# Optimization experiments

Measured on AMD Instinct MI355X. Metric: run time of the kernel, lower is better.

Reference implementation:

```python
import jax, jax.numpy as jnp
import numpy as np

NUM_VOCAB = 50000
EMBED_DIM = 128
SENT_SIZE = 50
MAX_HOPS = 3
BATCH = 128
MEM_SIZE = 200


def position_encoding(sentence_size, embedding_dim):
    # vectorized version of the original double loop
    i = np.arange(1, embedding_dim + 1, dtype=np.float32)[:, None]  # [D,1]
    j = np.arange(1, sentence_size + 1, dtype=np.float32)[None, :]  # [1,S]
    enc = (i - (embedding_dim + 1) / 2.0) * (j - (sentence_size + 1) / 2.0)
    enc = 1.0 + 4.0 * enc / embedding_dim / sentence_size
    enc[:, -1] = 1.0
    return np.transpose(enc).astype(np.float32)  # [S,D]


def setup_inputs() -> dict:
    key = jax.random.key(0)
    k1, k2, k3, k4, k5 = jax.random.split(key, 5)
    story = jax.random.randint(k1, (BATCH, MEM_SIZE, SENT_SIZE), 0, NUM_VOCAB, dtype=jnp.int64)
    query = jax.random.randint(k2, (BATCH, SENT_SIZE), 0, NUM_VOCAB, dtype=jnp.int64)
    # max_hops+1 embedding tables, N(0, 0.1), padding_idx=0 row zeroed
    C = 0.1 * jax.random.normal(k3, (MAX_HOPS + 1, NUM_VOCAB, EMBED_DIM), dtype=jnp.float32)
    C = C.at[:, 0, :].set(0.0)
    # T_k linear layer (PyTorch default uniform init bound)
    bound = 1.0 / np.sqrt(EMBED_DIM)
    T_w = jax.random.uniform(k4, (EMBED_DIM, EMBED_DIM), jnp.float32, -bound, bound)
    T_b = jax.random.uniform(k5, (EMBED_DIM,), jnp.float32, -bound, bound)
    return {"story": story, "query": query, "C": C, "T_w": T_w, "T_b": T_b}


def reference(story, query, C, T_w, T_b):
    enc = jnp.asarray(position_encoding(SENT_SIZE, EMBED_DIM))  # [S,D]
    # u0: position-encoded sum of query embedding
    q_emb = C[0][query]  # [B,S,D]
    u = jnp.einsum('bsd,sd->bd', q_emb, enc)
    for hop in range(MAX_HOPS):
        emb_A = C[hop][story]          # [B,M,S,D]
        m_A = jnp.einsum('bmsd,sd->bmd', emb_A, enc)
        prob = jax.nn.softmax(jnp.einsum('bmd,bd->bm', m_A, u), axis=-1)
        emb_C = C[hop + 1][story]      # [B,M,S,D]
        m_C = jnp.einsum('bmsd,sd->bmd', emb_C, enc)
        o_k = jnp.einsum('bmd,bm->bd', m_C, prob)
        t_k = jax.nn.sigmoid(u @ T_w.T + T_b)
        u = (1.0 - t_k) * u + o_k * t_k
    a_hat = u @ C[MAX_HOPS].T  # [B,V]
    return a_hat
```

## Files before the change

kernel.cpp:

```cpp
#include <hip/hip_runtime.h>
#include <cstdint>
#include <cstddef>

#define NV 50000
#define ED 128
#define SS 50
#define NB 128
#define NM 200
#define BMD (NB*NM*ED)
#define NCH 32
#define CHD 1563

typedef _Float16 f16x8 __attribute__((ext_vector_type(8)));
typedef _Float16 f16x4 __attribute__((ext_vector_type(4)));
typedef _Float16 f16x2 __attribute__((ext_vector_type(2)));
typedef float    f32x4 __attribute__((ext_vector_type(4)));

__global__ __launch_bounds__(256) void cvt_c3_k(
    const float* __restrict__ src, _Float16* __restrict__ dst) {
  const int i = blockIdx.x * 256 + threadIdx.x;
  const float4* s4 = (const float4*)src;
  float4 f0 = s4[2 * (size_t)i];
  float4 f1 = s4[2 * (size_t)i + 1];
  f16x8 h;
  h[0] = (_Float16)f0.x; h[1] = (_Float16)f0.y;
  h[2] = (_Float16)f0.z; h[3] = (_Float16)f0.w;
  h[4] = (_Float16)f1.x; h[5] = (_Float16)f1.y;
  h[6] = (_Float16)f1.z; h[7] = (_Float16)f1.w;
  *(f16x8*)(dst + (size_t)8 * i) = h;
}

__global__ __launch_bounds__(256) void story_embed_k(
    const int* __restrict__ story, const float* __restrict__ C,
    const _Float16* __restrict__ C3h, float* __restrict__ Mt) {
  const int wave = threadIdx.x >> 6;
  const int lane = threadIdx.x & 63;
  const int bm0 = blockIdx.x * 16;
  const int sl = (lane < SS) ? lane : (SS - 1);

  int idxg[4], cidg[4];
#pragma unroll
  for (int gg = 0; gg < 4; ++gg) {
    const int bm = bm0 + wave + 4 * gg;
    idxg[gg] = story[(size_t)bm * SS + sl];
    cidg[gg] = (lane < SS) ? (idxg[gg] / CHD) : -1;
  }
  const float a0 = ((float)(2*lane + 1) - 64.5f) * 6.25e-4f;
  const float a1 = ((float)(2*lane + 2) - 64.5f) * 6.25e-4f;
  float2 acc[4][4];
#pragma unroll
  for (int gg = 0; gg < 4; ++gg)
#pragma unroll
    for (int k = 0; k < 4; ++k) acc[gg][k] = make_float2(0.f, 0.f);

  for (int c = 0; c < NCH; ++c) {
#pragma unroll
    for (int gg = 0; gg < 4; ++gg) {
      unsigned long long mask = __ballot(cidg[gg] == c);
      while (mask) {
        const int s = __builtin_ctzll(mask);
        mask &= mask - 1;
        const int row = __shfl(idxg[gg], s);
        float e0, e1;
        if (s == SS - 1) { e0 = 1.0f; e1 = 1.0f; }
        else {
          float js = (float)(s + 1) - 25.5f;
          e0 = fmaf(a0, js, 1.0f);
          e1 = fmaf(a1, js, 1.0f);
        }
        const float* base = C + (size_t)row * ED + 2 * lane;
#pragma unroll
        for (int k = 0; k < 3; ++k) {
          float2 cv = *(const float2*)(base + (size_t)k * NV * ED);
          acc[gg][k].x = fmaf(e0, cv.x, acc[gg][k].x);
          acc[gg][k].y = fmaf(e1, cv.y, acc[gg][k].y);
        }
        f16x2 cv3 = *(const f16x2*)(C3h + (size_t)row * ED + 2 * lane);
        acc[gg][3].x = fmaf(e0, (float)cv3[0], acc[gg][3].x);
        acc[gg][3].y = fmaf(e1, (float)cv3[1], acc[gg][3].y);
      }
    }
    __syncthreads();
  }

#pragma unroll
  for (int gg = 0; gg < 4; ++gg) {
    const int bm = bm0 + wave + 4 * gg;
#pragma unroll
    for (int k = 0; k < 4; ++k)
      *(float2*)(Mt + (size_t)k * BMD + (size_t)bm * ED + 2 * lane) = acc[gg][k];
  }
}

__global__ __launch_bounds__(512, 2) void hops_k(
    const int* __restrict__ query, const float* __restrict__ C,
    const float* __restrict__ Tw, const float* __restrict__ Tb,
    const float* __restrict__ Mt, float* __restrict__ U) {
  const int b = blockIdx.x;
  const int tid = threadIdx.x;
  const int d = tid & 127;
  const int p = tid >> 7;
  const int wave = tid >> 6, lane = tid & 63;
  __shared__ float tile[NM * ED];
  __shared__ float u[ED];
  __shared__ float part[512];
  __shared__ float sc[NM];
  __shared__ float o[ED];

  {
    const float4* s4 = (const float4*)(Mt + (size_t)b * NM * ED);
    float4* t4 = (float4*)tile;
    float4 st[13];
#pragma unroll
    for (int j = 0; j < 13; ++j) {
      int i = tid + 512 * j;
      st[j] = (i < NM * ED / 4) ? s4[i] : make_float4(0.f, 0.f, 0.f, 0.f);
    }
#pragma unroll
    for (int j = 0; j < 13; ++j) {
      int i = tid + 512 * j;
      if (i < NM * ED / 4) t4[i] = st[j];
    }
  }

  {
    const float ad = ((float)(d + 1) - 64.5f) * 6.25e-4f;
    int rows[13];
#pragma unroll
    for (int j = 0; j < 13; ++j) {
      int s = p + 4 * j;
      rows[j] = query[b * SS + (s < SS ? s : 0)];
    }
    float cv[13];
#pragma unroll
    for (int j = 0; j < 13; ++j)
      cv[j] = C[(size_t)rows[j] * ED + d];
    float accv = 0.f;
#pragma unroll
    for (int j = 0; j < 13; ++j) {
      int s = p + 4 * j;
      float e;
      if (s >= SS) e = 0.f;
      else if (s == SS - 1) e = 1.0f;
      else e = fmaf(ad, (float)(s + 1) - 25.5f, 1.0f);
      accv = fmaf(e, cv[j], accv);
    }
    part[tid] = accv;
  }
  __syncthreads();
  if (tid < ED)
    u[tid] = part[tid] + part[tid + 128] + part[tid + 256] + part[tid + 384];
  __syncthreads();

  for (int hop = 0; hop < 3; ++hop) {
    const float* Tn = Mt + (size_t)(hop + 1) * BMD + (size_t)b * NM * ED;
    float pf[50];
#pragma unroll
    for (int j = 0; j < 50; ++j)
      pf[j] = Tn[(size_t)(p + 4 * j) * ED + d];

    {
      float u0v = u[2 * lane], u1v = u[2 * lane + 1];
      for (int m = wave; m < NM; m += 16) {
        const int m2 = m + 8;
        const bool has2 = (m2 < NM);
        float2 r0 = *(const float2*)&tile[m * ED + 2 * lane];
        float pa = r0.x * u0v + r0.y * u1v;
        float pb = 0.f;
        if (has2) {
          float2 r1 = *(const float2*)&tile[m2 * ED + 2 * lane];
          pb = r1.x * u0v + r1.y * u1v;
        }
#pragma unroll
        for (int off = 32; off; off >>= 1) {
          pa += __shfl_xor(pa, off);
          pb += __shfl_xor(pb, off);
        }
        if (lane == 0) {
          sc[m] = pa;
          if (has2) sc[m2] = pb;
        }
      }
    }
    __syncthreads();

    float v = (tid < NM) ? sc[tid] : -1e30f;
    {
      float t = v;
#pragma unroll
      for (int off = 32; off; off >>= 1) t = fmaxf(t, __shfl_xor(t, off));
      if (lane == 0) part[wave] = t;
    }
    __syncthreads();
    float mx = part[0];
#pragma unroll
    for (int w = 1; w < 8; ++w) mx = fmaxf(mx, part[w]);
    float ev = 0.f;
    if (tid < NM) { ev = __expf(v - mx); sc[tid] = ev; }
    {
      float t = ev;
#pragma unroll
      for (int off = 32; off; off >>= 1) t += __shfl_xor(t, off);
      if (lane == 0) part[8 + wave] = t;
    }
    __syncthreads();
    float tot = part[8];
#pragma unroll
    for (int w = 9; w < 16; ++w) tot += part[w];
    const float inv = 1.0f / tot;
    __syncthreads();

    {
      float oacc = 0.f;
#pragma unroll
      for (int j = 0; j < 50; ++j)
        oacc = fmaf(sc[p + 4 * j], pf[j], oacc);
      part[tid] = oacc;
    }
    if (hop < 2) {
#pragma unroll
      for (int j = 0; j < 50; ++j)
        tile[(p + 4 * j) * ED + d] = pf[j];
    }
    __syncthreads();
    if (tid < ED)
      o[tid] = (part[tid] + part[tid + 128] + part[tid + 256] + part[tid + 384])
               * inv;
    __syncthreads();

    {
      const float4* twr = (const float4*)(Tw + (size_t)d * ED + p * 32);
      float4 tw4[8];
#pragma unroll
      for (int j = 0; j < 8; ++j) tw4[j] = twr[j];
      float tacc = 0.f;
#pragma unroll
      for (int j = 0; j < 8; ++j) {
        tacc = fmaf(u[p * 32 + 4 * j + 0], tw4[j].x, tacc);
        tacc = fmaf(u[p * 32 + 4 * j + 1], tw4[j].y, tacc);
        tacc = fmaf(u[p * 32 + 4 * j + 2], tw4[j].z, tacc);
        tacc = fmaf(u[p * 32 + 4 * j + 3], tw4[j].w, tacc);
      }
      part[tid] = tacc;
    }
    __syncthreads();
    if (tid < ED) {
      float dot = part[tid] + part[tid + 128] + part[tid + 256] + part[tid + 384]
                  + Tb[tid];
      float tk = 1.0f / (1.0f + __expf(-dot));
      u[tid] = (1.0f - tk) * u[tid] + o[tid] * tk;
    }
    __syncthreads();
  }
  if (tid < ED) U[(size_t)b * ED + tid] = u[tid];
}

__global__ __launch_bounds__(256) void out_mm_mfma_k(
    const float* __restrict__ U, const _Float16* __restrict__ C3h,
    float* __restrict__ out) {
  __shared__ _Float16 Ub[ED * 136];
  const int tid = threadIdx.x;

  {
    const float4* u4 = (const float4*)U;
#pragma unroll
    for (int j = 0; j < 16; ++j) {
      int i = tid + 256 * j;
      float4 f = u4[i];
      int row = i >> 5;
      int col = (i & 31) * 4;
      f16x4 h;
      h[0] = (_Float16)f.x; h[1] = (_Float16)f.y;
      h[2] = (_Float16)f.z; h[3] = (_Float16)f.w;
      *(f16x4*)&Ub[row * 136 + col] = h;
    }
  }
  __syncthreads();

  const int wave = tid >> 6, lane = tid & 63;
  const int n = lane & 15, q = lane >> 4;
  const int v = blockIdx.x * 64 + wave * 16 + n;
  const bool vok = (v < NV);

  f32x4 acc[8];
#pragma unroll
  for (int mt = 0; mt < 8; ++mt) acc[mt] = (f32x4){0.f, 0.f, 0.f, 0.f};

#pragma unroll
  for (int kt = 0; kt < 4; ++kt) {
    f16x8 bfrag = {};
    if (vok) bfrag = *(const f16x8*)(C3h + (size_t)v * ED + kt * 32 + q * 8);
#pragma unroll
    for (int mt = 0; mt < 8; ++mt) {
      f16x8 afrag = *(const f16x8*)&Ub[(mt * 16 + n) * 136 + kt * 32 + q * 8];
      acc[mt] = __builtin_amdgcn_mfma_f32_16x16x32_f16(afrag, bfrag, acc[mt],
                                                       0, 0, 0);
    }
  }

  if (vok) {
#pragma unroll
    for (int mt = 0; mt < 8; ++mt)
#pragma unroll
      for (int i = 0; i < 4; ++i)
        out[(size_t)(mt * 16 + q * 4 + i) * NV + v] = acc[mt][i];
  }
}

extern "C" void kernel_launch(void* const* d_in, const int* in_sizes, int n_in,
                              void* d_out, int out_size, void* d_ws, size_t ws_size,
                              hipStream_t stream) {
  const int*   story = (const int*)d_in[0];
  const int*   query = (const int*)d_in[1];
  const float* C     = (const float*)d_in[2];
  const float* Tw    = (const float*)d_in[3];
  const float* Tb    = (const float*)d_in[4];
  float* out = (float*)d_out;

  float* wsf = (float*)d_ws;
  float*     Mt  = wsf;
  float*     U   = wsf + (size_t)4 * BMD;
  _Float16*  C3h = (_Float16*)(wsf + (size_t)4 * BMD + NB * ED);

  hipLaunchKernelGGL(cvt_c3_k, dim3(NV * ED / 8 / 256), dim3(256), 0, stream,
                     C + (size_t)3 * NV * ED, C3h);
  hipLaunchKernelGGL(story_embed_k, dim3(NB * NM / 16), dim3(256), 0, stream,
                     story, C, C3h, Mt);
  hipLaunchKernelGGL(hops_k, dim3(NB), dim3(512), 0, stream,
                     query, C, Tw, Tb, Mt, U);
  hipLaunchKernelGGL(out_mm_mfma_k, dim3((NV + 63) / 64), dim3(256), 0, stream,
                     U, C3h, out);
}
```

Measured before the change: 359.9 us.

## Process two gathered story rows per iteration and widen hops kernel to 1024 threads

The story embedding gather loop now pops two matching lanes from the ballot mask per iteration and issues both rows' loads before the FMAs, raising memory-level parallelism in this latency-bound gather. The hops kernel doubles its block to 1024 threads, halving per-thread register arrays (pf, tile staging) and the per-thread work in each reduction, with the partial sums now reduced over 8 slices. The cost is more register pressure in the gather loop and only one 1024-thread block per CU for hops, which has just 128 blocks anyway.

```diff
diff --git a/kernel.cpp b/kernel.cpp
--- a/kernel.cpp
+++ b/kernel.cpp
@@ -58,26 +58,48 @@
     for (int gg = 0; gg < 4; ++gg) {
       unsigned long long mask = __ballot(cidg[gg] == c);
       while (mask) {
-        const int s = __builtin_ctzll(mask);
+        const int s0 = __builtin_ctzll(mask);
         mask &= mask - 1;
-        const int row = __shfl(idxg[gg], s);
-        float e0, e1;
-        if (s == SS - 1) { e0 = 1.0f; e1 = 1.0f; }
+        const bool two = (mask != 0);
+        int s1 = s0;
+        if (two) { s1 = __builtin_ctzll(mask); mask &= mask - 1; }
+        const int row0 = __shfl(idxg[gg], s0);
+        const int row1 = __shfl(idxg[gg], s1);
+        float e00, e01, e10, e11;
+        if (s0 == SS - 1) { e00 = 1.0f; e01 = 1.0f; }
         else {
-          float js = (float)(s + 1) - 25.5f;
-          e0 = fmaf(a0, js, 1.0f);
-          e1 = fmaf(a1, js, 1.0f);
-        }
-        const float* base = C + (size_t)row * ED + 2 * lane;
+          float js = (float)(s0 + 1) - 25.5f;
+          e00 = fmaf(a0, js, 1.0f);
+          e01 = fmaf(a1, js, 1.0f);
+        }
+        if (!two) { e10 = 0.f; e11 = 0.f; }
+        else if (s1 == SS - 1) { e10 = 1.0f; e11 = 1.0f; }
+        else {
+          float js = (float)(s1 + 1) - 25.5f;
+          e10 = fmaf(a0, js, 1.0f);
+          e11 = fmaf(a1, js, 1.0f);
+        }
+        const float* b0 = C + (size_t)row0 * ED + 2 * lane;
+        const float* b1 = C + (size_t)row1 * ED + 2 * lane;
+        float2 cv0[3], cv1[3];
 #pragma unroll
         for (int k = 0; k < 3; ++k) {
-          float2 cv = *(const float2*)(base + (size_t)k * NV * ED);
-          acc[gg][k].x = fmaf(e0, cv.x, acc[gg][k].x);
-          acc[gg][k].y = fmaf(e1, cv.y, acc[gg][k].y);
-        }
-        f16x2 cv3 = *(const f16x2*)(C3h + (size_t)row * ED + 2 * lane);
-        acc[gg][3].x = fmaf(e0, (float)cv3[0], acc[gg][3].x);
-        acc[gg][3].y = fmaf(e1, (float)cv3[1], acc[gg][3].y);
+          cv0[k] = *(const float2*)(b0 + (size_t)k * NV * ED);
+          cv1[k] = *(const float2*)(b1 + (size_t)k * NV * ED);
+        }
+        f16x2 h0 = *(const f16x2*)(C3h + (size_t)row0 * ED + 2 * lane);
+        f16x2 h1 = *(const f16x2*)(C3h + (size_t)row1 * ED + 2 * lane);
+#pragma unroll
+        for (int k = 0; k < 3; ++k) {
+          acc[gg][k].x = fmaf(e00, cv0[k].x, acc[gg][k].x);
+          acc[gg][k].y = fmaf(e01, cv0[k].y, acc[gg][k].y);
+          acc[gg][k].x = fmaf(e10, cv1[k].x, acc[gg][k].x);
+          acc[gg][k].y = fmaf(e11, cv1[k].y, acc[gg][k].y);
+        }
+        acc[gg][3].x = fmaf(e00, (float)h0[0], acc[gg][3].x);
+        acc[gg][3].y = fmaf(e01, (float)h0[1], acc[gg][3].y);
+        acc[gg][3].x = fmaf(e10, (float)h1[0], acc[gg][3].x);
+        acc[gg][3].y = fmaf(e11, (float)h1[1], acc[gg][3].y);
       }
     }
     __syncthreads();
@@ -92,7 +114,7 @@
   }
 }
 
-__global__ __launch_bounds__(512, 2) void hops_k(
+__global__ __launch_bounds__(1024, 1) void hops_k(
     const int* __restrict__ query, const float* __restrict__ C,
     const float* __restrict__ Tw, const float* __restrict__ Tb,
     const float* __restrict__ Mt, float* __restrict__ U) {
@@ -103,42 +125,42 @@
   const int wave = tid >> 6, lane = tid & 63;
   __shared__ float tile[NM * ED];
   __shared__ float u[ED];
-  __shared__ float part[512];
+  __shared__ float part[1024];
   __shared__ float sc[NM];
   __shared__ float o[ED];
 
   {
     const float4* s4 = (const float4*)(Mt + (size_t)b * NM * ED);
     float4* t4 = (float4*)tile;
-    float4 st[13];
-#pragma unroll
-    for (int j = 0; j < 13; ++j) {
-      int i = tid + 512 * j;
-      st[j] = (i < NM * ED / 4) ? s4[i] : make_float4(0.f, 0.f, 0.f, 0.f);
-    }
-#pragma unroll
-    for (int j = 0; j < 13; ++j) {
-      int i = tid + 512 * j;
+    float4 st[7];
+#pragma unroll
+    for (int j = 0; j < 7; ++j) {
+      int i = tid + 1024 * j;
+      if (i < NM * ED / 4) st[j] = s4[i];
+    }
+#pragma unroll
+    for (int j = 0; j < 7; ++j) {
+      int i = tid + 1024 * j;
       if (i < NM * ED / 4) t4[i] = st[j];
     }
   }
 
   {
     const float ad = ((float)(d + 1) - 64.5f) * 6.25e-4f;
-    int rows[13];
-#pragma unroll
-    for (int j = 0; j < 13; ++j) {
-      int s = p + 4 * j;
+    int rows[7];
+#pragma unroll
+    for (int j = 0; j < 7; ++j) {
+      int s = p + 8 * j;
       rows[j] = query[b * SS + (s < SS ? s : 0)];
     }
-    float cv[13];
-#pragma unroll
-    for (int j = 0; j < 13; ++j)
+    float cv[7];
+#pragma unroll
+    for (int j = 0; j < 7; ++j)
       cv[j] = C[(size_t)rows[j] * ED + d];
     float accv = 0.f;
 #pragma unroll
-    for (int j = 0; j < 13; ++j) {
-      int s = p + 4 * j;
+    for (int j = 0; j < 7; ++j) {
+      int s = p + 8 * j;
       float e;
       if (s >= SS) e = 0.f;
       else if (s == SS - 1) e = 1.0f;
@@ -148,21 +170,25 @@
     part[tid] = accv;
   }
   __syncthreads();
-  if (tid < ED)
-    u[tid] = part[tid] + part[tid + 128] + part[tid + 256] + part[tid + 384];
+  if (tid < ED) {
+    float s = 0.f;
+#pragma unroll
+    for (int k = 0; k < 8; ++k) s += part[tid + 128 * k];
+    u[tid] = s;
+  }
   __syncthreads();
 
   for (int hop = 0; hop < 3; ++hop) {
     const float* Tn = Mt + (size_t)(hop + 1) * BMD + (size_t)b * NM * ED;
-    float pf[50];
-#pragma unroll
-    for (int j = 0; j < 50; ++j)
-      pf[j] = Tn[(size_t)(p + 4 * j) * ED + d];
+    float pf[25];
+#pragma unroll
+    for (int j = 0; j < 25; ++j)
+      pf[j] = Tn[(size_t)(p + 8 * j) * ED + d];
 
     {
       float u0v = u[2 * lane], u1v = u[2 * lane + 1];
-      for (int m = wave; m < NM; m += 16) {
-        const int m2 = m + 8;
+      for (int m = wave; m < NM; m += 32) {
+        const int m2 = m + 16;
         const bool has2 = (m2 < NM);
         float2 r0 = *(const float2*)&tile[m * ED + 2 * lane];
         float pa = r0.x * u0v + r0.y * u1v;
@@ -194,59 +220,63 @@
     __syncthreads();
     float mx = part[0];
 #pragma unroll
-    for (int w = 1; w < 8; ++w) mx = fmaxf(mx, part[w]);
+    for (int w = 1; w < 16; ++w) mx = fmaxf(mx, part[w]);
     float ev = 0.f;
     if (tid < NM) { ev = __expf(v - mx); sc[tid] = ev; }
     {
       float t = ev;
 #pragma unroll
       for (int off = 32; off; off >>= 1) t += __shfl_xor(t, off);
-      if (lane == 0) part[8 + wave] = t;
-    }
-    __syncthreads();
-    float tot = part[8];
-#pragma unroll
-    for (int w = 9; w < 16; ++w) tot += part[w];
+      if (lane == 0) part[16 + wave] = t;
+    }
+    __syncthreads();
+    float tot = part[16];
+#pragma unroll
+    for (int w = 17; w < 32; ++w) tot += part[w];
     const float inv = 1.0f / tot;
     __syncthreads();
 
     {
       float oacc = 0.f;
 #pragma unroll
-      for (int j = 0; j < 50; ++j)
-        oacc = fmaf(sc[p + 4 * j], pf[j], oacc);
+      for (int j = 0; j < 25; ++j)
+        oacc = fmaf(sc[p + 8 * j], pf[j], oacc);
       part[tid] = oacc;
     }
     if (hop < 2) {
 #pragma unroll
-      for (int j = 0; j < 50; ++j)
-        tile[(p + 4 * j) * ED + d] = pf[j];
-    }
-    __syncthreads();
-    if (tid < ED)
-      o[tid] = (part[tid] + part[tid + 128] + part[tid + 256] + part[tid + 384])
-               * inv;
-    __syncthreads();
-
-    {
-      const float4* twr = (const float4*)(Tw + (size_t)d * ED + p * 32);
-      float4 tw4[8];
-#pragma unroll
-      for (int j = 0; j < 8; ++j) tw4[j] = twr[j];
+      for (int j = 0; j < 25; ++j)
+        tile[(p + 8 * j) * ED + d] = pf[j];
+    }
+    __syncthreads();
+    if (tid < ED) {
+      float s = 0.f;
+#pragma unroll
+      for (int k = 0; k < 8; ++k) s += part[tid + 128 * k];
+      o[tid] = s * inv;
+    }
+    __syncthreads();
+
+    {
+      const float4* twr = (const float4*)(Tw + (size_t)d * ED + p * 16);
+      float4 tw4[4];
+#pragma unroll
+      for (int j = 0; j < 4; ++j) tw4[j] = twr[j];
       float tacc = 0.f;
 #pragma unroll
-      for (int j = 0; j < 8; ++j) {
-        tacc = fmaf(u[p * 32 + 4 * j + 0], tw4[j].x, tacc);
-        tacc = fmaf(u[p * 32 + 4 * j + 1], tw4[j].y, tacc);
-        tacc = fmaf(u[p * 32 + 4 * j + 2], tw4[j].z, tacc);
-        tacc = fmaf(u[p * 32 + 4 * j + 3], tw4[j].w, tacc);
+      for (int j = 0; j < 4; ++j) {
+        tacc = fmaf(u[p * 16 + 4 * j + 0], tw4[j].x, tacc);
+        tacc = fmaf(u[p * 16 + 4 * j + 1], tw4[j].y, tacc);
+        tacc = fmaf(u[p * 16 + 4 * j + 2], tw4[j].z, tacc);
+        tacc = fmaf(u[p * 16 + 4 * j + 3], tw4[j].w, tacc);
       }
       part[tid] = tacc;
     }
     __syncthreads();
     if (tid < ED) {
-      float dot = part[tid] + part[tid + 128] + part[tid + 256] + part[tid + 384]
-                  + Tb[tid];
+      float dot = Tb[tid];
+#pragma unroll
+      for (int k = 0; k < 8; ++k) dot += part[tid + 128 * k];
       float tk = 1.0f / (1.0f + __expf(-dot));
       u[tid] = (1.0f - tk) * u[tid] + o[tid] * tk;
     }
@@ -326,7 +356,7 @@
                      C + (size_t)3 * NV * ED, C3h);
   hipLaunchKernelGGL(story_embed_k, dim3(NB * NM / 16), dim3(256), 0, stream,
                      story, C, C3h, Mt);
-  hipLaunchKernelGGL(hops_k, dim3(NB), dim3(512), 0, stream,
+  hipLaunchKernelGGL(hops_k, dim3(NB), dim3(1024), 0, stream,
                      query, C, Tw, Tb, Mt, U);
   hipLaunchKernelGGL(out_mm_mfma_k, dim3((NV + 63) / 64), dim3(256), 0, stream,
                      U, C3h, out);
```

After: 473.9 us. 31.7% more time.
